# Optimization experiments

Hardware: AMD Instinct MI355X
Metric: run time of the kernel (lower is better)

## Reference

```python
import jax, jax.numpy as jnp
import numpy as np

N_NODES = 100000


def setup_inputs() -> dict:
    key = jax.random.key(0)
    k1, k2, k3 = jax.random.split(key, 3)
    X = jax.random.normal(k1, (N_NODES, 128), dtype=jnp.float32)
    W = jax.random.normal(k2, (128, 128), dtype=jnp.float32) * (1.0 / np.sqrt(128))
    edge_index = jax.random.randint(k3, (2, 1600000), 0, N_NODES, dtype=jnp.int64)
    return {"X": X, "W": W, "edge_index": edge_index}


def reference(X, W, edge_index):
    # GCNConv: out = D_hat^{-1/2} (A + I) D_hat^{-1/2} @ (X W^T)
    N = X.shape[0]
    row, col = edge_index[0], edge_index[1]
    # A_hat = A + I : append self-loop edges
    loops = jnp.arange(N, dtype=row.dtype)
    row_h = jnp.concatenate([row, loops])
    col_h = jnp.concatenate([col, loops])
    # D_hat = A_hat.sum(0): column sums -> degree indexed by col
    deg = jax.ops.segment_sum(jnp.ones(col_h.shape[0], dtype=X.dtype), col_h,
                              num_segments=N)
    d_invsqrt = deg ** -0.5  # deg >= 1 due to self loops
    # edge value of H = D^-1/2 A_hat D^-1/2
    val = d_invsqrt[row_h] * d_invsqrt[col_h]  # [E+N]
    # linear projection (nn.Linear, no bias): X @ W^T
    X_hat = X @ W.T  # [N, out]
    # SpMM (sum): out[r] += val * X_hat[c]
    msgs = val[:, None] * X_hat[col_h]  # [E+N, out]
    return jax.ops.segment_sum(msgs, row_h, num_segments=N)
```

## Files before the change

kernel.cpp:

```cpp
#include <hip/hip_runtime.h>
#include <hip/hip_bf16.h>
#include <stdint.h>

typedef __bf16 bf16_t;
typedef bf16_t bf16x8 __attribute__((ext_vector_type(8)));
typedef bf16_t bf16x2 __attribute__((ext_vector_type(2)));
typedef float  f32x4  __attribute__((ext_vector_type(4)));
typedef float  f32x2  __attribute__((ext_vector_type(2)));

#define N_FEAT 128
#define NBMAX  196
#define BINB   512

__global__ void detect_k(const int* __restrict__ edges, int* __restrict__ flag) {
    int v = edges[2 * threadIdx.x + 1];
    unsigned long long m = __ballot(v != 0);
    if (threadIdx.x == 0) *flag = (m == 0ull) ? 1 : 0;
}
__device__ inline int eread(const int* __restrict__ edges, int f, long i) {
    return f ? edges[2 * i] : edges[i];
}

__device__ inline int detect_inline(const int* __restrict__ edges, int* sh) {
    if (threadIdx.x < 64) {
        int v = edges[2 * threadIdx.x + 1];
        unsigned long long m = __ballot(v != 0);
        if (threadIdx.x == 0) sh[0] = (m == 0ull) ? 1 : 0;
    }
    __syncthreads();
    return sh[0];
}

__device__ inline bf16x8 cvt8(const float* __restrict__ p) {
    f32x4 lo = *(const f32x4*)p;
    f32x4 hi = *(const f32x4*)(p + 4);
    bf16x8 r;
    r[0] = (bf16_t)lo[0]; r[1] = (bf16_t)lo[1]; r[2] = (bf16_t)lo[2]; r[3] = (bf16_t)lo[3];
    r[4] = (bf16_t)hi[0]; r[5] = (bf16_t)hi[1]; r[6] = (bf16_t)hi[2]; r[7] = (bf16_t)hi[3];
    return r;
}

__device__ inline int block_scan_incl(int v, int* wsum ) {
    const int t = threadIdx.x, lane = t & 63, wid = t >> 6;
    int x = v;
#pragma unroll
    for (int off = 1; off < 64; off <<= 1) {
        int y = __shfl_up(x, off);
        if (lane >= off) x += y;
    }
    if (lane == 63) wsum[wid] = x;
    __syncthreads();
    int add = 0;
    for (int w = 0; w < wid; ++w) add += wsum[w];
    return x + add;
}

__global__ __launch_bounds__(64) void gemm_xwts(const float* __restrict__ X,
                                                const bf16_t* __restrict__ Wbf,
                                                const float* __restrict__ dinv,
                                                bf16_t* __restrict__ Xhat) {
    const int lane = threadIdx.x;
    const int m  = lane & 15;
    const int kq = lane >> 4;
    const long r0 = (long)blockIdx.x * 16;

    f32x4 acc[8];
#pragma unroll
    for (int c = 0; c < 8; ++c) acc[c] = (f32x4){0.f, 0.f, 0.f, 0.f};

    const float* xrow = X + (r0 + m) * N_FEAT + kq * 8;
#pragma unroll
    for (int kb = 0; kb < 4; ++kb) {
        bf16x8 a = cvt8(xrow + kb * 32);
#pragma unroll
        for (int c = 0; c < 8; ++c) {
            bf16x8 b = *(const bf16x8*)(Wbf + (c * 16 + m) * N_FEAT + kb * 32 + kq * 8);
            acc[c] = __builtin_amdgcn_mfma_f32_16x16x32_bf16(a, b, acc[c], 0, 0, 0);
        }
    }
    float dr[4];
#pragma unroll
    for (int i = 0; i < 4; ++i) dr[i] = dinv[r0 + kq * 4 + i];
#pragma unroll
    for (int c = 0; c < 8; ++c) {
#pragma unroll
        for (int i = 0; i < 4; ++i) {
            long r = r0 + kq * 4 + i;
            Xhat[r * N_FEAT + c * 16 + m] = (bf16_t)(dr[i] * acc[c][i]);
        }
    }
}


__global__ __launch_bounds__(256) void bin_k(const int* __restrict__ edges,
                                             int E, int N, int NB,
                                             int* __restrict__ hist,
                                             const float* __restrict__ W,
                                             bf16_t* __restrict__ Wbf,
                                             bf16_t* __restrict__ xpad) {
    const int bid = blockIdx.x;
    if (bid >= BINB) {
        const int b2 = bid - BINB;
        if (b2 < 64) {
            int i = b2 * 256 + threadIdx.x;
            Wbf[i] = (bf16_t)W[i];
        } else if (threadIdx.x < N_FEAT) {
            xpad[threadIdx.x] = (bf16_t)0.0f;
        }
        return;
    }
    __shared__ int h[2 * NBMAX];
    __shared__ int shf[1];
    const int f = detect_inline(edges, shf);
    const int nb2 = 2 * NB;
    for (int j = threadIdx.x; j < nb2; j += 256) h[j] = 0;
    __syncthreads();
    const int chunk = (E + BINB - 1) / BINB;
    const int e0 = bid * chunk, e1 = min(E, e0 + chunk);
    if (f) {
        const int2* e2 = (const int2*)edges;
        for (int e = e0 + (int)threadIdx.x; e < e1; e += 256) {
            int r = e2[e].x, c = e2[(long)E + e].x;
            if ((unsigned)r < (unsigned)N && (unsigned)c < (unsigned)N) {
                atomicAdd(&h[r >> 9], 1);
                atomicAdd(&h[NB + (c >> 9)], 1);
            }
        }
    } else {
        for (int e = e0 + (int)threadIdx.x; e < e1; e += 256) {
            int r = edges[e], c = edges[(long)E + e];
            if ((unsigned)r < (unsigned)N && (unsigned)c < (unsigned)N) {
                atomicAdd(&h[r >> 9], 1);
                atomicAdd(&h[NB + (c >> 9)], 1);
            }
        }
    }
    __syncthreads();
    for (int j = threadIdx.x; j < nb2; j += 256) hist[(long)j * BINB + bid] = h[j];
}

__global__ __launch_bounds__(BINB) void scan_k(const int* __restrict__ hist, int NB,
                                               int* __restrict__ baseTab,
                                               int* __restrict__ totals) {
    __shared__ int wsum[BINB / 64];
    const int j = blockIdx.x;
    const int t = threadIdx.x;
    int v = hist[(long)j * BINB + t];
    int incl = block_scan_incl(v, wsum);
    baseTab[(long)j * BINB + t] = incl - v;
    if (t == BINB - 1) totals[j] = incl;
}

__global__ __launch_bounds__(512) void bucketbase_k(const int* __restrict__ totals,
                                                    int NB, int N,
                                                    int* __restrict__ famBase,
                                                    int* __restrict__ start) {
    __shared__ int wsum[8];
    __shared__ int sh_tot0;
    const int t = threadIdx.x;
    const int nb2 = 2 * NB;
    int v = (t < nb2) ? totals[t] : 0;
    int incl = block_scan_incl(v, wsum);
    int excl = incl - v;
    if (t == NB) sh_tot0 = excl;
    __syncthreads();
    if (t < NB) famBase[t] = excl;
    if (t == NB) { famBase[NB] = excl; start[N] = excl; }
    if (t >= NB && t < nb2) famBase[NB + 1 + (t - NB)] = excl - sh_tot0;
    if (t == nb2 - 1) famBase[NB + 1 + NB] = incl - sh_tot0;
}

__global__ __launch_bounds__(256) void bscatter_k(const int* __restrict__ edges,
                                                  int E, int N, int NB,
                                                  const int* __restrict__ baseTab,
                                                  const int* __restrict__ famBase,
                                                  unsigned* __restrict__ rowbuf,
                                                  int* __restrict__ colbuf) {
    __shared__ int cur[2 * NBMAX];
    __shared__ int shf[1];
    const int f = detect_inline(edges, shf);
    const int blk = blockIdx.x;
    const int nb2 = 2 * NB;
    for (int j = threadIdx.x; j < nb2; j += 256) {
        int fb = (j < NB) ? famBase[j] : famBase[NB + 1 + (j - NB)];
        cur[j] = fb + baseTab[(long)j * BINB + blk];
    }
    __syncthreads();
    const int chunk = (E + BINB - 1) / BINB;
    const int e0 = blk * chunk, e1 = min(E, e0 + chunk);
    if (f) {
        const int2* e2 = (const int2*)edges;
        for (int e = e0 + (int)threadIdx.x; e < e1; e += 256) {
            int r = e2[e].x, c = e2[(long)E + e].x;
            if ((unsigned)r < (unsigned)N && (unsigned)c < (unsigned)N) {
                int pr = atomicAdd(&cur[r >> 9], 1);
                rowbuf[pr] = ((unsigned)(r & 511) << 17) | (unsigned)c;
                int pc = atomicAdd(&cur[NB + (c >> 9)], 1);
                colbuf[pc] = c & 511;
            }
        }
    } else {
        for (int e = e0 + (int)threadIdx.x; e < e1; e += 256) {
            int r = edges[e], c = edges[(long)E + e];
            if ((unsigned)r < (unsigned)N && (unsigned)c < (unsigned)N) {
                int pr = atomicAdd(&cur[r >> 9], 1);
                rowbuf[pr] = ((unsigned)(r & 511) << 17) | (unsigned)c;
                int pc = atomicAdd(&cur[NB + (c >> 9)], 1);
                colbuf[pc] = c & 511;
            }
        }
    }
}

__global__ __launch_bounds__(512) void degcsr_k(const unsigned* __restrict__ rowbuf,
                                                const int* __restrict__ colbuf,
                                                const int* __restrict__ famBase,
                                                int NB, int N,
                                                int* __restrict__ start,
                                                int* __restrict__ ecol,
                                                float* __restrict__ dinv) {
    __shared__ int cnt[512];
    __shared__ int wsum[8];
    const int t = threadIdx.x;
    if ((int)blockIdx.x >= NB) {
        const int b = blockIdx.x - NB;
        cnt[t] = 0;
        __syncthreads();
        const int e0 = famBase[NB + 1 + b], e1 = famBase[NB + 1 + b + 1];
        for (int e = e0 + t; e < e1; e += 512)
            atomicAdd(&cnt[colbuf[e]], 1);
        __syncthreads();
        int n = (b << 9) + t;
        if (n < N) dinv[n] = rsqrtf((float)(cnt[t] + 1));
        return;
    }
    const int b = blockIdx.x;
    cnt[t] = 0;
    __syncthreads();
    const int e0 = famBase[b], e1 = famBase[b + 1];
    for (int e = e0 + t; e < e1; e += 512)
        atomicAdd(&cnt[rowbuf[e] >> 17], 1);
    __syncthreads();
    int v = cnt[t];
    int incl = block_scan_incl(v, wsum);
    int excl = incl - v;
    const int n = (b << 9) + t;
    if (n < N) start[n] = e0 + excl;
    cnt[t] = e0 + excl;
    __syncthreads();
    for (int e = e0 + t; e < e1; e += 512) {
        unsigned w = rowbuf[e];
        int pos = atomicAdd(&cnt[w >> 17], 1);
        ecol[pos] = (int)(w & 0x1FFFFu);
    }
}

__global__ __launch_bounds__(64) void gather6_k(const int* __restrict__ ecol,
                                                const int* __restrict__ start,
                                                const float* __restrict__ dinv,
                                                const bf16_t* __restrict__ Xhat,
                                                int N,
                                                float* __restrict__ out) {
    const int n = blockIdx.x;
    const int j = threadIdx.x;
    const int s = start[n], e = start[n + 1];

    bf16x2 xs = *(const bf16x2*)(Xhat + (long)n * N_FEAT + 2 * j);
    float a0 = (float)xs[0];
    float a1 = (float)xs[1];

    for (int p = s; p < e; p += 16) {
        int cq[16];
#pragma unroll
        for (int q = 0; q < 16; ++q) {
            int tt = p + q;
            int idx = (tt < e) ? tt : s;
            int cc = ecol[idx];
            cq[q] = (tt < e) ? cc : N;
        }
#pragma unroll
        for (int q = 0; q < 16; ++q) {
            bf16x2 xv = *(const bf16x2*)(Xhat + (long)cq[q] * N_FEAT + 2 * j);
            a0 += (float)xv[0];
            a1 += (float)xv[1];
        }
    }
    const float dn = dinv[n];
    f32x2 o; o[0] = dn * a0; o[1] = dn * a1;
    *(f32x2*)(out + (long)n * N_FEAT + 2 * j) = o;
}


__global__ __launch_bounds__(64) void gemm_xwt(const float* __restrict__ X,
                                               const float* __restrict__ W,
                                               bf16_t* __restrict__ Xhat) {
    const int lane = threadIdx.x;
    const int m  = lane & 15;
    const int kq = lane >> 4;
    const long r0 = (long)blockIdx.x * 16;
    f32x4 acc[8];
#pragma unroll
    for (int c = 0; c < 8; ++c) acc[c] = (f32x4){0.f, 0.f, 0.f, 0.f};
    const float* xrow = X + (r0 + m) * N_FEAT + kq * 8;
#pragma unroll
    for (int kb = 0; kb < 4; ++kb) {
        bf16x8 a = cvt8(xrow + kb * 32);
#pragma unroll
        for (int c = 0; c < 8; ++c) {
            bf16x8 b = cvt8(W + (c * 16 + m) * N_FEAT + kb * 32 + kq * 8);
            acc[c] = __builtin_amdgcn_mfma_f32_16x16x32_bf16(a, b, acc[c], 0, 0, 0);
        }
    }
#pragma unroll
    for (int c = 0; c < 8; ++c)
#pragma unroll
        for (int i = 0; i < 4; ++i) {
            long r = r0 + kq * 4 + i;
            Xhat[r * N_FEAT + c * 16 + m] = (bf16_t)acc[c][i];
        }
}

__global__ void degree_k(const int* __restrict__ edges, const int* __restrict__ flag,
                         int E, int N,
                         int* __restrict__ cnt_row, int* __restrict__ cnt_col) {
    int e = blockIdx.x * blockDim.x + threadIdx.x;
    int f = *flag;
    if (e < E) {
        int r = eread(edges, f, e);
        int c = eread(edges, f, (long)E + e);
        if ((unsigned)r < (unsigned)N) atomicAdd(&cnt_row[r], 1);
        if ((unsigned)c < (unsigned)N) atomicAdd(&cnt_col[c], 1);
    }
}

__global__ void degree_col_k(const int* __restrict__ edges, const int* __restrict__ flag,
                             int E, int N, int* __restrict__ cnt_col) {
    int e = blockIdx.x * blockDim.x + threadIdx.x;
    int f = *flag;
    if (e < E) {
        int c = eread(edges, f, (long)E + e);
        if ((unsigned)c < (unsigned)N) atomicAdd(&cnt_col[c], 1);
    }
}

__global__ void alloc_k(const int* __restrict__ cnt_row, int N,
                        int* __restrict__ cur, int* __restrict__ total,
                        int* cnt_col_in, float* dinv_out) {
    int n = blockIdx.x * blockDim.x + threadIdx.x;
    if (n < N) {
        cur[n] = atomicAdd(total, cnt_row[n]);
        int dc = cnt_col_in[n];
        dinv_out[n] = rsqrtf((float)(dc + 1));
    }
}

__global__ void scatter_k(const int* __restrict__ edges, const int* __restrict__ flag,
                          int E, int N, int* __restrict__ cur, int* __restrict__ ecol) {
    int e = blockIdx.x * blockDim.x + threadIdx.x;
    int f = *flag;
    if (e < E) {
        int r = eread(edges, f, e);
        if ((unsigned)r < (unsigned)N) {
            int p = atomicAdd(&cur[r], 1);
            if ((unsigned)p < (unsigned)E)
                ecol[p] = eread(edges, f, (long)E + e);
        }
    }
}

__global__ __launch_bounds__(64) void gather_k(const int* __restrict__ ecol,
                                               const int* __restrict__ cur,
                                               const int* __restrict__ cnt_row,
                                               const float* __restrict__ dinv,
                                               const bf16_t* __restrict__ Xhat,
                                               int N,
                                               float* __restrict__ out) {
    const int n = blockIdx.x;
    const int j = threadIdx.x;
    const int c = cnt_row[n];
    const int s = cur[n] - c;
    const float dn = dinv[n];
    bf16x2 xs = *(const bf16x2*)(Xhat + (long)n * N_FEAT + 2 * j);
    float a0 = dn * (float)xs[0];
    float a1 = dn * (float)xs[1];
    for (int e = 0; e < c; ++e) {
        int cc = ecol[s + e];
        if ((unsigned)cc >= (unsigned)N) continue;
        float dc = dinv[cc];
        bf16x2 xv = *(const bf16x2*)(Xhat + (long)cc * N_FEAT + 2 * j);
        a0 += dc * (float)xv[0];
        a1 += dc * (float)xv[1];
    }
    f32x2 o; o[0] = dn * a0; o[1] = dn * a1;
    *(f32x2*)(out + (long)n * N_FEAT + 2 * j) = o;
}


__global__ __launch_bounds__(128) void self_k(const int* __restrict__ cnt_col,
                                              const bf16_t* __restrict__ Xhat,
                                              float* __restrict__ out) {
    const int n = blockIdx.x;
    const int j = threadIdx.x;
    const float dn2 = 1.0f / (float)(cnt_col[n] + 1);
    out[(long)n * N_FEAT + j] = dn2 * (float)Xhat[(long)n * N_FEAT + j];
}

__global__ __launch_bounds__(128) void edge_add_k(const int* __restrict__ edges,
                                                  const int* __restrict__ flag,
                                                  int E, int N,
                                                  const int* __restrict__ cnt_col,
                                                  const bf16_t* __restrict__ Xhat,
                                                  float* __restrict__ out) {
    const int e = blockIdx.x;
    const int j = threadIdx.x;
    int f = *flag;
    const int r = eread(edges, f, e);
    const int c = eread(edges, f, (long)E + e);
    if ((unsigned)r >= (unsigned)N || (unsigned)c >= (unsigned)N) return;
    const float val = rsqrtf((float)(cnt_col[r] + 1)) * rsqrtf((float)(cnt_col[c] + 1));
    atomicAdd(&out[(long)r * N_FEAT + j], val * (float)Xhat[(long)c * N_FEAT + j]);
}

extern "C" void kernel_launch(void* const* d_in, const int* in_sizes, int n_in,
                              void* d_out, int out_size, void* d_ws, size_t ws_size,
                              hipStream_t stream) {
    const float* X = (const float*)d_in[0];
    const float* W = (const float*)d_in[1];
    const int* edges = (const int*)d_in[2];
    const int E = in_sizes[2] / 2;
    const int N = in_sizes[0] / N_FEAT;
    const int NB = (N + 511) >> 9;

    char* ws = (char*)d_ws;
    const size_t xhat_b = (size_t)(N + 1) * N_FEAT * sizeof(bf16_t);
    const size_t n4     = (size_t)N * 4;
    auto al = [](size_t x) { return (x + 255) & ~(size_t)255; };

    size_t off = 0;
    int*      flag   = (int*)(ws + off);        off = 256;
    bf16_t*   Wbf    = (bf16_t*)(ws + off);     off = al(off + 128 * 128 * 2);
    bf16_t*   Xhat   = (bf16_t*)(ws + off);     off = al(off + xhat_b);
    float*    dinv   = (float*)(ws + off);      off = al(off + n4);
    int*      startA = (int*)(ws + off);        off = al(off + n4 + 4);
    unsigned* rowbuf = (unsigned*)(ws + off);   off = al(off + (size_t)E * 4);
    int*      colbuf = (int*)(ws + off);        off = al(off + (size_t)E * 4);
    int*      ecol   = (int*)(ws + off);        off = al(off + (size_t)E * 4);
    int*      hist   = (int*)(ws + off);        off = al(off + (size_t)BINB * 2 * NB * 4);
    int*      baseTab= (int*)(ws + off);        off = al(off + (size_t)BINB * 2 * NB * 4);
    int*      totals = (int*)(ws + off);        off = al(off + (size_t)(2 * NB) * 4);
    int*      famBase= (int*)(ws + off);        off = al(off + (size_t)(2 * NB + 2) * 4);
    const size_t need_S = off;

    int* cnt_col = (int*)(ws + 16 + xhat_b);
    const size_t need_A = 16 + xhat_b + n4 * 3 + 16 + (size_t)E * 4;
    const size_t need_B = 16 + xhat_b + n4;

    if (ws_size >= need_S && NB <= NBMAX && N <= 100352 && (N & 15) == 0 && E >= BINB) {
        bin_k<<<BINB + 65, 256, 0, stream>>>(edges, E, N, NB, hist,
                                             W, Wbf, Xhat + (size_t)N * N_FEAT);
        scan_k<<<2 * NB, BINB, 0, stream>>>(hist, NB, baseTab, totals);
        bucketbase_k<<<1, 512, 0, stream>>>(totals, NB, N, famBase, startA);
        bscatter_k<<<BINB, 256, 0, stream>>>(edges, E, N, NB, baseTab, famBase,
                                             rowbuf, colbuf);
        degcsr_k<<<2 * NB, 512, 0, stream>>>(rowbuf, colbuf, famBase, NB, N,
                                             startA, ecol, dinv);
        gemm_xwts<<<N / 16, 64, 0, stream>>>(X, Wbf, dinv, Xhat);
        gather6_k<<<N, 64, 0, stream>>>(ecol, startA, dinv, Xhat, N, (float*)d_out);
    } else if (ws_size >= need_A) {
        bf16_t* XhatA  = (bf16_t*)(ws + 16);
        int*   cnt_row = (int*)(ws + 16 + xhat_b + n4);
        int*   cur     = (int*)(ws + 16 + xhat_b + n4 * 2);
        int*   total   = (int*)(ws + 16 + xhat_b + n4 * 3);
        int*   ecolA   = (int*)(ws + 16 + xhat_b + n4 * 3 + 16);
        float* dinvA   = (float*)cnt_col;

        hipMemsetAsync(cnt_col, 0, n4 * 2, stream);
        hipMemsetAsync(total, 0, 16, stream);
        detect_k<<<1, 64, 0, stream>>>(edges, flag);
        gemm_xwt<<<N / 16, 64, 0, stream>>>(X, W, XhatA);
        degree_k<<<(E + 255) / 256, 256, 0, stream>>>(edges, flag, E, N, cnt_row, cnt_col);
        alloc_k<<<(N + 255) / 256, 256, 0, stream>>>(cnt_row, N, cur, total, cnt_col, dinvA);
        scatter_k<<<(E + 255) / 256, 256, 0, stream>>>(edges, flag, E, N, cur, ecolA);
        gather_k<<<N, 64, 0, stream>>>(ecolA, cur, cnt_row, dinvA, XhatA, N, (float*)d_out);
    } else if (ws_size >= need_B) {
        bf16_t* XhatB = (bf16_t*)(ws + 16);
        hipMemsetAsync(cnt_col, 0, n4, stream);
        detect_k<<<1, 64, 0, stream>>>(edges, flag);
        gemm_xwt<<<N / 16, 64, 0, stream>>>(X, W, XhatB);
        degree_col_k<<<(E + 255) / 256, 256, 0, stream>>>(edges, flag, E, N, cnt_col);
        self_k<<<N, 128, 0, stream>>>(cnt_col, XhatB, (float*)d_out);
        edge_add_k<<<E, 128, 0, stream>>>(edges, flag, E, N, cnt_col, XhatB, (float*)d_out);
    }
}
```

Before: 242.3 us.

## Split column-degree pass and co-schedule GEMM tiles with row CSR build

Column-degree computation moves into its own kernel. The row CSR construction and the X·Wᵀ GEMM tiles are merged into one launch, so the GEMM blocks can overlap with the row-bucket work instead of running as a separate kernel afterward. The scan kernel now uses a strided mapping when reading the histogram, and the gather loop batch drops from 16 to 8 indices. The cost is one extra launch for column degrees, plus the risk of mixed block sizes and less memory-level parallelism in the gather.

```diff
diff --git a/kernel.cpp b/kernel.cpp
--- a/kernel.cpp
+++ b/kernel.cpp
@@ -55,19 +55,16 @@
     return x + add;
 }
 
-__global__ __launch_bounds__(64) void gemm_xwts(const float* __restrict__ X,
-                                                const bf16_t* __restrict__ Wbf,
-                                                const float* __restrict__ dinv,
-                                                bf16_t* __restrict__ Xhat) {
-    const int lane = threadIdx.x;
+__device__ inline void gemm_tile_s(long tile, const float* __restrict__ X,
+                                   const bf16_t* __restrict__ Wbf,
+                                   const float* __restrict__ dinv,
+                                   bf16_t* __restrict__ Xhat, int lane) {
     const int m  = lane & 15;
     const int kq = lane >> 4;
-    const long r0 = (long)blockIdx.x * 16;
-
+    const long r0 = tile * 16;
     f32x4 acc[8];
 #pragma unroll
     for (int c = 0; c < 8; ++c) acc[c] = (f32x4){0.f, 0.f, 0.f, 0.f};
-
     const float* xrow = X + (r0 + m) * N_FEAT + kq * 8;
 #pragma unroll
     for (int kb = 0; kb < 4; ++kb) {
@@ -82,13 +79,12 @@
 #pragma unroll
     for (int i = 0; i < 4; ++i) dr[i] = dinv[r0 + kq * 4 + i];
 #pragma unroll
-    for (int c = 0; c < 8; ++c) {
+    for (int c = 0; c < 8; ++c)
 #pragma unroll
         for (int i = 0; i < 4; ++i) {
             long r = r0 + kq * 4 + i;
             Xhat[r * N_FEAT + c * 16 + m] = (bf16_t)(dr[i] * acc[c][i]);
         }
-    }
 }
 
 
@@ -145,9 +141,10 @@
     __shared__ int wsum[BINB / 64];
     const int j = blockIdx.x;
     const int t = threadIdx.x;
-    int v = hist[(long)j * BINB + t];
+    const int b = ((t & 63) << 3) | (t >> 6);
+    int v = hist[(long)j * BINB + b];
     int incl = block_scan_incl(v, wsum);
-    baseTab[(long)j * BINB + t] = incl - v;
+    baseTab[(long)j * BINB + b] = incl - v;
     if (t == BINB - 1) totals[j] = incl;
 }
 
@@ -212,29 +209,42 @@
     }
 }
 
-__global__ __launch_bounds__(512) void degcsr_k(const unsigned* __restrict__ rowbuf,
-                                                const int* __restrict__ colbuf,
+__global__ __launch_bounds__(512) void coldeg_k(const int* __restrict__ colbuf,
                                                 const int* __restrict__ famBase,
                                                 int NB, int N,
-                                                int* __restrict__ start,
-                                                int* __restrict__ ecol,
                                                 float* __restrict__ dinv) {
     __shared__ int cnt[512];
+    const int t = threadIdx.x;
+    const int b = blockIdx.x;
+    cnt[t] = 0;
+    __syncthreads();
+    const int e0 = famBase[NB + 1 + b], e1 = famBase[NB + 1 + b + 1];
+    for (int e = e0 + t; e < e1; e += 512)
+        atomicAdd(&cnt[colbuf[e]], 1);
+    __syncthreads();
+    int n = (b << 9) + t;
+    if (n < N) dinv[n] = rsqrtf((float)(cnt[t] + 1));
+}
+
+__global__ __launch_bounds__(512) void rowgemm_k(const unsigned* __restrict__ rowbuf,
+                                                 const int* __restrict__ famBase,
+                                                 int NB, int N, int ntiles,
+                                                 int* __restrict__ start,
+                                                 int* __restrict__ ecol,
+                                                 const float* __restrict__ X,
+                                                 const bf16_t* __restrict__ Wbf,
+                                                 const float* __restrict__ dinv,
+                                                 bf16_t* __restrict__ Xhat) {
+    const int t = threadIdx.x;
+    const int bid = blockIdx.x;
+    if (bid >= NB) {
+        const long tile = (long)(bid - NB) * 8 + (t >> 6);
+        if (tile < ntiles) gemm_tile_s(tile, X, Wbf, dinv, Xhat, t & 63);
+        return;
+    }
+    __shared__ int cnt[512];
     __shared__ int wsum[8];
-    const int t = threadIdx.x;
-    if ((int)blockIdx.x >= NB) {
-        const int b = blockIdx.x - NB;
-        cnt[t] = 0;
-        __syncthreads();
-        const int e0 = famBase[NB + 1 + b], e1 = famBase[NB + 1 + b + 1];
-        for (int e = e0 + t; e < e1; e += 512)
-            atomicAdd(&cnt[colbuf[e]], 1);
-        __syncthreads();
-        int n = (b << 9) + t;
-        if (n < N) dinv[n] = rsqrtf((float)(cnt[t] + 1));
-        return;
-    }
-    const int b = blockIdx.x;
+    const int b = bid;
     cnt[t] = 0;
     __syncthreads();
     const int e0 = famBase[b], e1 = famBase[b + 1];
@@ -255,7 +265,7 @@
     }
 }
 
-__global__ __launch_bounds__(64) void gather6_k(const int* __restrict__ ecol,
+__global__ __launch_bounds__(64) void gather5_k(const int* __restrict__ ecol,
                                                 const int* __restrict__ start,
                                                 const float* __restrict__ dinv,
                                                 const bf16_t* __restrict__ Xhat,
@@ -269,17 +279,17 @@
     float a0 = (float)xs[0];
     float a1 = (float)xs[1];
 
-    for (int p = s; p < e; p += 16) {
-        int cq[16];
-#pragma unroll
-        for (int q = 0; q < 16; ++q) {
+    for (int p = s; p < e; p += 8) {
+        int cq[8];
+#pragma unroll
+        for (int q = 0; q < 8; ++q) {
             int tt = p + q;
             int idx = (tt < e) ? tt : s;
             int cc = ecol[idx];
             cq[q] = (tt < e) ? cc : N;
         }
 #pragma unroll
-        for (int q = 0; q < 16; ++q) {
+        for (int q = 0; q < 8; ++q) {
             bf16x2 xv = *(const bf16x2*)(Xhat + (long)cq[q] * N_FEAT + 2 * j);
             a0 += (float)xv[0];
             a1 += (float)xv[1];
@@ -456,16 +466,18 @@
     const size_t need_B = 16 + xhat_b + n4;
 
     if (ws_size >= need_S && NB <= NBMAX && N <= 100352 && (N & 15) == 0 && E >= BINB) {
+        const int ntiles = N / 16;
+        const int GEMMB  = (ntiles + 7) / 8;
         bin_k<<<BINB + 65, 256, 0, stream>>>(edges, E, N, NB, hist,
                                              W, Wbf, Xhat + (size_t)N * N_FEAT);
         scan_k<<<2 * NB, BINB, 0, stream>>>(hist, NB, baseTab, totals);
         bucketbase_k<<<1, 512, 0, stream>>>(totals, NB, N, famBase, startA);
         bscatter_k<<<BINB, 256, 0, stream>>>(edges, E, N, NB, baseTab, famBase,
                                              rowbuf, colbuf);
-        degcsr_k<<<2 * NB, 512, 0, stream>>>(rowbuf, colbuf, famBase, NB, N,
-                                             startA, ecol, dinv);
-        gemm_xwts<<<N / 16, 64, 0, stream>>>(X, Wbf, dinv, Xhat);
-        gather6_k<<<N, 64, 0, stream>>>(ecol, startA, dinv, Xhat, N, (float*)d_out);
+        coldeg_k<<<NB, 512, 0, stream>>>(colbuf, famBase, NB, N, dinv);
+        rowgemm_k<<<NB + GEMMB, 512, 0, stream>>>(rowbuf, famBase, NB, N, ntiles,
+                                                  startA, ecol, X, Wbf, dinv, Xhat);
+        gather5_k<<<N, 64, 0, stream>>>(ecol, startA, dinv, Xhat, N, (float*)d_out);
     } else if (ws_size >= need_A) {
         bf16_t* XhatA  = (bf16_t*)(ws + 16);
         int*   cnt_row = (int*)(ws + 16 + xhat_b + n4);
```

Result: no change. 242.4 us (+0.0%).
